# Performance work log

Measured on AMD Instinct MI355X. Metric: run time of the kernel, lower is better.

Reference implementation:

```python
import jax, jax.numpy as jnp
import numpy as np

IMAGE_DIM = 224


def setup_inputs() -> dict:
    key = jax.random.key(0)
    k1, k2, k3, k4, k5 = jax.random.split(key, 5)
    N, H, W = 64, IMAGE_DIM, IMAGE_DIM
    im1 = jax.random.normal(k1, (N, 3, H, W), dtype=jnp.float32)
    im2 = jax.random.normal(k2, (N, 3, H, W), dtype=jnp.float32)
    C = jax.random.normal(k3, (N, 2, H, W), dtype=jnp.float32)
    M1 = jax.random.uniform(k4, (N, 1, H, W), dtype=jnp.float32)
    M2 = jax.random.uniform(k5, (N, 1, H, W), dtype=jnp.float32)
    return {"im1": im1, "im2": im2, "C": C, "M1": M1, "M2": M2}


def _grid(dtype):
    # q = [repeat(arange(H), W), tile(arange(W), H)], shape [2, H*W]
    x = jnp.repeat(jnp.arange(IMAGE_DIM), IMAGE_DIM)
    y = jnp.tile(jnp.arange(IMAGE_DIM), IMAGE_DIM)
    return jnp.stack([x, y]).astype(dtype)  # [2, HW]


def _bilinear_sample(imflat, qi):
    # imflat: [N, 3, HW], qi: [N, 2, HW] float coords
    HW = imflat.shape[-1]
    px, py = qi[:, 0], qi[:, 1]  # [N, HW]
    fx, cx = jnp.floor(px), jnp.ceil(px)
    fy, cy = jnp.floor(py), jnp.ceil(py)

    def gather_pixel(nx, ny):
        # weight = prod over axes of (1 - |point - neighbor|)
        w = (1.0 - jnp.abs(px - nx)) * (1.0 - jnp.abs(py - ny))  # [N, HW]
        ind = (nx + IMAGE_DIM * ny).astype(jnp.int32)
        ind = jnp.clip(ind, 0, HW - 1)  # guard against out-of-range neighbors
        pix = jnp.take_along_axis(imflat, ind[:, None, :], axis=2)  # [N, 3, HW]
        return w[:, None, :] * pix

    return (gather_pixel(fx, fy) + gather_pixel(cx, fy)
            + gather_pixel(fx, cy) + gather_pixel(cy * 0 + cx, cy))


def reference(im1, im2, C, M1, M2):
    N, ch, H, W = im1.shape
    HW = H * W
    q = _grid(im1.dtype)[None]              # [1, 2, HW]
    Cflat = C.reshape(N, 2, HW)
    a = _bilinear_sample(im1.reshape(N, ch, HW), q + Cflat).reshape(N, ch, H, W) * M1
    b = _bilinear_sample(im2.reshape(N, ch, HW), q - Cflat).reshape(N, ch, H, W) * M2
    return a + b
```

## Files before the change

### kernel.cpp

```cpp
#include <hip/hip_runtime.h>

#define IMG 224
#define HW (IMG * IMG)
#define TILE 32
#define PAD 4
#define REG (TILE + 2 * PAD)
#define RSA 41
#define TABA (REG * RSA)
#define RSB 44
#define TABB (REG * RSB)

#define NXCD 8
#define NWG  (49 * 64)

typedef float vfloat4 __attribute__((ext_vector_type(4)));

__global__ __launch_bounds__(256, 4) void vm_kernel(
    const float* __restrict__ im1, const float* __restrict__ im2,
    const float* __restrict__ C, const float* __restrict__ M1,
    const float* __restrict__ M2, float* __restrict__ out)
{
    __shared__ float2 tabA[2 * TABA];
    __shared__ float  tabB[2 * TABB];

    const int bid     = blockIdx.x;
    const int logical = (bid & (NXCD - 1)) * (NWG / NXCD) + (bid >> 3);
    const int n       = logical / 49;
    const int tile    = logical - n * 49;

    const int x0   = (tile / 7) * TILE;
    const int y0   = (tile % 7) * TILE;
    const int t    = threadIdx.x;
    const int xlo  = x0 - PAD;
    const int ylo  = y0 - PAD;
    const int gbase = xlo + IMG * ylo;

    const float* i1n = im1 + (size_t)n * 3 * HW;
    const float* i2n = im2 + (size_t)n * 3 * HW;
    const float* Cn  = C  + (size_t)n * 2 * HW;
    const float* M1n = M1 + (size_t)n * HW;
    const float* M2n = M2 + (size_t)n * HW;

#pragma unroll
    for (int img = 0; img < 2; ++img) {
        const float* src = img ? i2n : i1n;
        float2* TA = tabA + img * TABA;
        float*  TB = tabB + img * TABB;
#pragma unroll
        for (int k = 0; k < 2; ++k) {
            int e = t + 256 * k;
            if (e < 400) {
                int r = e / 10, s = e - r * 10;
                int gi = gbase + IMG * r + 4 * s;
                float4 a, b, c;
                if (gi >= 0 && gi <= HW - 4) {
                    a = *(const float4*)(src + gi);
                    b = *(const float4*)(src + HW + gi);
                    c = *(const float4*)(src + 2 * HW + gi);
                } else {
#pragma unroll
                    for (int i = 0; i < 4; ++i) {
                        int g = min(max(gi + i, 0), HW - 1);
                        ((float*)&a)[i] = src[g];
                        ((float*)&b)[i] = src[HW + g];
                        ((float*)&c)[i] = src[2 * HW + g];
                    }
                }
                float2* dA = TA + r * RSA + 4 * s;
                dA[0] = make_float2(a.x, b.x);
                dA[1] = make_float2(a.y, b.y);
                dA[2] = make_float2(a.z, b.z);
                dA[3] = make_float2(a.w, b.w);
                *(float4*)(TB + r * RSB + 4 * s) = c;
            }
        }
    }

    const int tx  = t >> 3;
    const int ty0 = (t & 7) * 4;
    const int p   = (x0 + tx) * IMG + (y0 + ty0);

    const vfloat4 c0v = __builtin_nontemporal_load((const vfloat4*)(Cn + p));
    const vfloat4 c1v = __builtin_nontemporal_load((const vfloat4*)(Cn + HW + p));
    const vfloat4 m1v = __builtin_nontemporal_load((const vfloat4*)(M1n + p));
    const vfloat4 m2v = __builtin_nontemporal_load((const vfloat4*)(M2n + p));

    __syncthreads();

    const float xf = (float)(x0 + tx);
    float acc0[4], acc1[4], acc2[4];

#pragma unroll
    for (int i = 0; i < 4; ++i) {
        const float yf  = (float)(y0 + ty0 + i);
        const float cc0 = c0v[i];
        const float cc1 = c1v[i];
        const float m1i = m1v[i];
        const float m2i = m2v[i];
        float r0c, r1c, r2c;

        {
            float px = xf + cc0, py = yf + cc1;
            float fx = floorf(px), cx = ceilf(px);
            float fy = floorf(py), cy = ceilf(py);
            float wfx = 1.0f - (px - fx), wcx = 1.0f - (cx - px);
            float wfy = 1.0f - (py - fy), wcy = 1.0f - (cy - py);
            float w0 = wfx * wfy, w1 = wcx * wfy;
            float w2 = wfx * wcy, w3 = wcx * wcy;
            int gx0 = (int)fx, gy0 = (int)fy;
            int dx = (int)cx - gx0, dy = (int)cy - gy0;
            int q0 = gx0 - xlo, r0 = gy0 - ylo;
            int in = (q0 >= 0) & (q0 + dx <= REG - 1) &
                     (r0 >= 0) & (r0 + dy <= REG - 1);
            if (__all(in)) {
                int oA = r0 * RSA + q0;
                int oB = r0 * RSB + q0;
                float2 a0 = tabA[oA],            a1 = tabA[oA + dx];
                float2 a2 = tabA[oA + dy * RSA], a3 = tabA[oA + dx + dy * RSA];
                float  b0 = tabB[oB],            b1 = tabB[oB + dx];
                float  b2 = tabB[oB + dy * RSB], b3 = tabB[oB + dx + dy * RSB];
                r0c = m1i * (w0 * a0.x + w1 * a1.x + w2 * a2.x + w3 * a3.x);
                r1c = m1i * (w0 * a0.y + w1 * a1.y + w2 * a2.y + w3 * a3.y);
                r2c = m1i * (w0 * b0   + w1 * b1   + w2 * b2   + w3 * b3);
            } else {
                int i0 = min(max(gx0      + IMG * gy0,        0), HW - 1);
                int i1 = min(max(gx0 + dx + IMG * gy0,        0), HW - 1);
                int i2 = min(max(gx0      + IMG * (gy0 + dy), 0), HW - 1);
                int i3 = min(max(gx0 + dx + IMG * (gy0 + dy), 0), HW - 1);
                r0c = m1i * (w0 * i1n[i0] + w1 * i1n[i1] +
                             w2 * i1n[i2] + w3 * i1n[i3]);
                r1c = m1i * (w0 * i1n[HW + i0] + w1 * i1n[HW + i1] +
                             w2 * i1n[HW + i2] + w3 * i1n[HW + i3]);
                r2c = m1i * (w0 * i1n[2 * HW + i0] + w1 * i1n[2 * HW + i1] +
                             w2 * i1n[2 * HW + i2] + w3 * i1n[2 * HW + i3]);
            }
        }
        {
            float px = xf - cc0, py = yf - cc1;
            float fx = floorf(px), cx = ceilf(px);
            float fy = floorf(py), cy = ceilf(py);
            float wfx = 1.0f - (px - fx), wcx = 1.0f - (cx - px);
            float wfy = 1.0f - (py - fy), wcy = 1.0f - (cy - py);
            float w0 = wfx * wfy, w1 = wcx * wfy;
            float w2 = wfx * wcy, w3 = wcx * wcy;
            int gx0 = (int)fx, gy0 = (int)fy;
            int dx = (int)cx - gx0, dy = (int)cy - gy0;
            int q0 = gx0 - xlo, r0 = gy0 - ylo;
            int in = (q0 >= 0) & (q0 + dx <= REG - 1) &
                     (r0 >= 0) & (r0 + dy <= REG - 1);
            if (__all(in)) {
                const float2* TA = tabA + TABA;
                const float*  TB = tabB + TABB;
                int oA = r0 * RSA + q0;
                int oB = r0 * RSB + q0;
                float2 a0 = TA[oA],            a1 = TA[oA + dx];
                float2 a2 = TA[oA + dy * RSA], a3 = TA[oA + dx + dy * RSA];
                float  b0 = TB[oB],            b1 = TB[oB + dx];
                float  b2 = TB[oB + dy * RSB], b3 = TB[oB + dx + dy * RSB];
                r0c += m2i * (w0 * a0.x + w1 * a1.x + w2 * a2.x + w3 * a3.x);
                r1c += m2i * (w0 * a0.y + w1 * a1.y + w2 * a2.y + w3 * a3.y);
                r2c += m2i * (w0 * b0   + w1 * b1   + w2 * b2   + w3 * b3);
            } else {
                int i0 = min(max(gx0      + IMG * gy0,        0), HW - 1);
                int i1 = min(max(gx0 + dx + IMG * gy0,        0), HW - 1);
                int i2 = min(max(gx0      + IMG * (gy0 + dy), 0), HW - 1);
                int i3 = min(max(gx0 + dx + IMG * (gy0 + dy), 0), HW - 1);
                r0c += m2i * (w0 * i2n[i0] + w1 * i2n[i1] +
                              w2 * i2n[i2] + w3 * i2n[i3]);
                r1c += m2i * (w0 * i2n[HW + i0] + w1 * i2n[HW + i1] +
                              w2 * i2n[HW + i2] + w3 * i2n[HW + i3]);
                r2c += m2i * (w0 * i2n[2 * HW + i0] + w1 * i2n[2 * HW + i1] +
                              w2 * i2n[2 * HW + i2] + w3 * i2n[2 * HW + i3]);
            }
        }
        acc0[i] = r0c; acc1[i] = r1c; acc2[i] = r2c;
    }

    float* on = out + (size_t)n * 3 * HW;
    vfloat4 s0 = {acc0[0], acc0[1], acc0[2], acc0[3]};
    vfloat4 s1 = {acc1[0], acc1[1], acc1[2], acc1[3]};
    vfloat4 s2 = {acc2[0], acc2[1], acc2[2], acc2[3]};
    __builtin_nontemporal_store(s0, (vfloat4*)(on + p));
    __builtin_nontemporal_store(s1, (vfloat4*)(on + HW + p));
    __builtin_nontemporal_store(s2, (vfloat4*)(on + 2 * HW + p));
}

extern "C" void kernel_launch(void* const* d_in, const int* in_sizes, int n_in,
                              void* d_out, int out_size, void* d_ws, size_t ws_size,
                              hipStream_t stream) {
    const float* im1 = (const float*)d_in[0];
    const float* im2 = (const float*)d_in[1];
    const float* C   = (const float*)d_in[2];
    const float* M1  = (const float*)d_in[3];
    const float* M2  = (const float*)d_in[4];
    float* out = (float*)d_out;
    vm_kernel<<<dim3(NWG), 256, 0, stream>>>(im1, im2, C, M1, M2, out);
}
```

Before: 171.0 us.

## Process two tiles per block, prefetching second tile's loads during first compute

Each block now handles two consecutive tiles. The global loads for the second tile are issued into registers before the first tile is computed, then written to shared memory after a barrier, so memory latency overlaps with compute. The grid is halved and launch bounds drop to 3 waves per SIMD to make room for the extra registers the prefetch needs. The cost is higher register pressure, an extra barrier, and fewer blocks to cover the GPU.

After: 172.9 us. No clear change (+1.2%).

```diff
diff --git a/kernel.cpp b/kernel.cpp
--- a/kernel.cpp
+++ b/kernel.cpp
@@ -12,81 +12,47 @@
 
 #define NXCD 8
 #define NWG  (49 * 64)
+#define NBLK (NWG / 2)
 
 typedef float vfloat4 __attribute__((ext_vector_type(4)));
 
-__global__ __launch_bounds__(256, 4) void vm_kernel(
-    const float* __restrict__ im1, const float* __restrict__ im2,
-    const float* __restrict__ C, const float* __restrict__ M1,
-    const float* __restrict__ M2, float* __restrict__ out)
+struct Unit { float4 a, b, c; };
+
+__device__ __forceinline__ Unit load_unit(const float* __restrict__ src, int gi) {
+    Unit u;
+    if (gi >= 0 && gi <= HW - 4) {
+        u.a = *(const float4*)(src + gi);
+        u.b = *(const float4*)(src + HW + gi);
+        u.c = *(const float4*)(src + 2 * HW + gi);
+    } else {
+#pragma unroll
+        for (int i = 0; i < 4; ++i) {
+            int g = min(max(gi + i, 0), HW - 1);
+            ((float*)&u.a)[i] = src[g];
+            ((float*)&u.b)[i] = src[HW + g];
+            ((float*)&u.c)[i] = src[2 * HW + g];
+        }
+    }
+    return u;
+}
+
+__device__ __forceinline__ void write_unit(float2* TA, float* TB,
+                                           int r, int s, const Unit& u) {
+    float2* dA = TA + r * RSA + 4 * s;
+    dA[0] = make_float2(u.a.x, u.b.x);
+    dA[1] = make_float2(u.a.y, u.b.y);
+    dA[2] = make_float2(u.a.z, u.b.z);
+    dA[3] = make_float2(u.a.w, u.b.w);
+    *(float4*)(TB + r * RSB + 4 * s) = u.c;
+}
+
+__device__ __forceinline__ void compute_tile(
+    int x0, int y0, int xlo, int ylo, int tx, int ty0, int p,
+    const float2* __restrict__ tabA, const float* __restrict__ tabB,
+    vfloat4 c0v, vfloat4 c1v, vfloat4 m1v, vfloat4 m2v,
+    const float* __restrict__ i1n, const float* __restrict__ i2n,
+    float* __restrict__ on)
 {
-    __shared__ float2 tabA[2 * TABA];
-    __shared__ float  tabB[2 * TABB];
-
-    const int bid     = blockIdx.x;
-    const int logical = (bid & (NXCD - 1)) * (NWG / NXCD) + (bid >> 3);
-    const int n       = logical / 49;
-    const int tile    = logical - n * 49;
-
-    const int x0   = (tile / 7) * TILE;
-    const int y0   = (tile % 7) * TILE;
-    const int t    = threadIdx.x;
-    const int xlo  = x0 - PAD;
-    const int ylo  = y0 - PAD;
-    const int gbase = xlo + IMG * ylo;
-
-    const float* i1n = im1 + (size_t)n * 3 * HW;
-    const float* i2n = im2 + (size_t)n * 3 * HW;
-    const float* Cn  = C  + (size_t)n * 2 * HW;
-    const float* M1n = M1 + (size_t)n * HW;
-    const float* M2n = M2 + (size_t)n * HW;
-
-#pragma unroll
-    for (int img = 0; img < 2; ++img) {
-        const float* src = img ? i2n : i1n;
-        float2* TA = tabA + img * TABA;
-        float*  TB = tabB + img * TABB;
-#pragma unroll
-        for (int k = 0; k < 2; ++k) {
-            int e = t + 256 * k;
-            if (e < 400) {
-                int r = e / 10, s = e - r * 10;
-                int gi = gbase + IMG * r + 4 * s;
-                float4 a, b, c;
-                if (gi >= 0 && gi <= HW - 4) {
-                    a = *(const float4*)(src + gi);
-                    b = *(const float4*)(src + HW + gi);
-                    c = *(const float4*)(src + 2 * HW + gi);
-                } else {
-#pragma unroll
-                    for (int i = 0; i < 4; ++i) {
-                        int g = min(max(gi + i, 0), HW - 1);
-                        ((float*)&a)[i] = src[g];
-                        ((float*)&b)[i] = src[HW + g];
-                        ((float*)&c)[i] = src[2 * HW + g];
-                    }
-                }
-                float2* dA = TA + r * RSA + 4 * s;
-                dA[0] = make_float2(a.x, b.x);
-                dA[1] = make_float2(a.y, b.y);
-                dA[2] = make_float2(a.z, b.z);
-                dA[3] = make_float2(a.w, b.w);
-                *(float4*)(TB + r * RSB + 4 * s) = c;
-            }
-        }
-    }
-
-    const int tx  = t >> 3;
-    const int ty0 = (t & 7) * 4;
-    const int p   = (x0 + tx) * IMG + (y0 + ty0);
-
-    const vfloat4 c0v = __builtin_nontemporal_load((const vfloat4*)(Cn + p));
-    const vfloat4 c1v = __builtin_nontemporal_load((const vfloat4*)(Cn + HW + p));
-    const vfloat4 m1v = __builtin_nontemporal_load((const vfloat4*)(M1n + p));
-    const vfloat4 m2v = __builtin_nontemporal_load((const vfloat4*)(M2n + p));
-
-    __syncthreads();
-
     const float xf = (float)(x0 + tx);
     float acc0[4], acc1[4], acc2[4];
 
@@ -176,13 +142,105 @@
         acc0[i] = r0c; acc1[i] = r1c; acc2[i] = r2c;
     }
 
-    float* on = out + (size_t)n * 3 * HW;
     vfloat4 s0 = {acc0[0], acc0[1], acc0[2], acc0[3]};
     vfloat4 s1 = {acc1[0], acc1[1], acc1[2], acc1[3]};
     vfloat4 s2 = {acc2[0], acc2[1], acc2[2], acc2[3]};
     __builtin_nontemporal_store(s0, (vfloat4*)(on + p));
     __builtin_nontemporal_store(s1, (vfloat4*)(on + HW + p));
     __builtin_nontemporal_store(s2, (vfloat4*)(on + 2 * HW + p));
+}
+
+__global__ __launch_bounds__(256, 3) void vm_kernel(
+    const float* __restrict__ im1, const float* __restrict__ im2,
+    const float* __restrict__ C, const float* __restrict__ M1,
+    const float* __restrict__ M2, float* __restrict__ out)
+{
+    __shared__ float2 tabA[2 * TABA];
+    __shared__ float  tabB[2 * TABB];
+
+    const int bid = blockIdx.x;
+    const int swz = (bid & (NXCD - 1)) * (NBLK / NXCD) + (bid >> 3);
+    const int l0  = swz * 2;
+
+    const int t    = threadIdx.x;
+    const int tx   = t >> 3;
+    const int ty0  = (t & 7) * 4;
+    const bool has1 = (t < 144);
+    const int r0u = t / 10,         s0u = t - r0u * 10;
+    const int r1u = (t + 256) / 10, s1u = (t + 256) - r1u * 10;
+
+    const int n0  = l0 / 49, tl0 = l0 - n0 * 49;
+    const int x00 = (tl0 / 7) * TILE, y00 = (tl0 % 7) * TILE;
+    const int xlo0 = x00 - PAD, ylo0 = y00 - PAD;
+    const int gb0  = xlo0 + IMG * ylo0;
+    const float* i1n0 = im1 + (size_t)n0 * 3 * HW;
+    const float* i2n0 = im2 + (size_t)n0 * 3 * HW;
+    const float* Cn0  = C   + (size_t)n0 * 2 * HW;
+    const int p0 = (x00 + tx) * IMG + (y00 + ty0);
+
+    Unit u1a = load_unit(i1n0, gb0 + IMG * r0u + 4 * s0u);
+    Unit u2a = load_unit(i2n0, gb0 + IMG * r0u + 4 * s0u);
+    Unit u1b, u2b;
+    if (has1) {
+        u1b = load_unit(i1n0, gb0 + IMG * r1u + 4 * s1u);
+        u2b = load_unit(i2n0, gb0 + IMG * r1u + 4 * s1u);
+    }
+    const vfloat4 c0v0 = __builtin_nontemporal_load((const vfloat4*)(Cn0 + p0));
+    const vfloat4 c1v0 = __builtin_nontemporal_load((const vfloat4*)(Cn0 + HW + p0));
+    const vfloat4 m1v0 = __builtin_nontemporal_load(
+        (const vfloat4*)(M1 + (size_t)n0 * HW + p0));
+    const vfloat4 m2v0 = __builtin_nontemporal_load(
+        (const vfloat4*)(M2 + (size_t)n0 * HW + p0));
+
+    write_unit(tabA, tabB, r0u, s0u, u1a);
+    write_unit(tabA + TABA, tabB + TABB, r0u, s0u, u2a);
+    if (has1) {
+        write_unit(tabA, tabB, r1u, s1u, u1b);
+        write_unit(tabA + TABA, tabB + TABB, r1u, s1u, u2b);
+    }
+    __syncthreads();
+
+    const int l1  = l0 + 1;
+    const int n1  = l1 / 49, tl1 = l1 - n1 * 49;
+    const int x01 = (tl1 / 7) * TILE, y01 = (tl1 % 7) * TILE;
+    const int xlo1 = x01 - PAD, ylo1 = y01 - PAD;
+    const int gb1  = xlo1 + IMG * ylo1;
+    const float* i1n1 = im1 + (size_t)n1 * 3 * HW;
+    const float* i2n1 = im2 + (size_t)n1 * 3 * HW;
+    const float* Cn1  = C   + (size_t)n1 * 2 * HW;
+    const int p1 = (x01 + tx) * IMG + (y01 + ty0);
+
+    Unit v1a = load_unit(i1n1, gb1 + IMG * r0u + 4 * s0u);
+    Unit v2a = load_unit(i2n1, gb1 + IMG * r0u + 4 * s0u);
+    Unit v1b, v2b;
+    if (has1) {
+        v1b = load_unit(i1n1, gb1 + IMG * r1u + 4 * s1u);
+        v2b = load_unit(i2n1, gb1 + IMG * r1u + 4 * s1u);
+    }
+    const vfloat4 c0v1 = __builtin_nontemporal_load((const vfloat4*)(Cn1 + p1));
+    const vfloat4 c1v1 = __builtin_nontemporal_load((const vfloat4*)(Cn1 + HW + p1));
+    const vfloat4 m1v1 = __builtin_nontemporal_load(
+        (const vfloat4*)(M1 + (size_t)n1 * HW + p1));
+    const vfloat4 m2v1 = __builtin_nontemporal_load(
+        (const vfloat4*)(M2 + (size_t)n1 * HW + p1));
+
+    compute_tile(x00, y00, xlo0, ylo0, tx, ty0, p0, tabA, tabB,
+                 c0v0, c1v0, m1v0, m2v0, i1n0, i2n0,
+                 out + (size_t)n0 * 3 * HW);
+
+    __syncthreads();
+
+    write_unit(tabA, tabB, r0u, s0u, v1a);
+    write_unit(tabA + TABA, tabB + TABB, r0u, s0u, v2a);
+    if (has1) {
+        write_unit(tabA, tabB, r1u, s1u, v1b);
+        write_unit(tabA + TABA, tabB + TABB, r1u, s1u, v2b);
+    }
+    __syncthreads();
+
+    compute_tile(x01, y01, xlo1, ylo1, tx, ty0, p1, tabA, tabB,
+                 c0v1, c1v1, m1v1, m2v1, i1n1, i2n1,
+                 out + (size_t)n1 * 3 * HW);
 }
 
 extern "C" void kernel_launch(void* const* d_in, const int* in_sizes, int n_in,
@@ -194,5 +252,5 @@
     const float* M1  = (const float*)d_in[3];
     const float* M2  = (const float*)d_in[4];
     float* out = (float*)d_out;
-    vm_kernel<<<dim3(NWG), 256, 0, stream>>>(im1, im2, C, M1, M2, out);
-}
+    vm_kernel<<<dim3(NBLK), 256, 0, stream>>>(im1, im2, C, M1, M2, out);
+}
```

## Precompute gather offsets before barrier and software-pipeline LDS bilinear reads

Applied to the files above, without the earlier changes.

Moves the C/M loads ahead of the tile staging and computes all eight sample offsets and wave-uniform in-tile flags before the barrier, so that index math overlaps with global loads. After the barrier, LDS gathers for the next pixel are issued before the current pixel's weights are combined, which double-buffers the shared-memory reads. This raises register pressure (offset arrays plus two Gath sets in flight) under launch bounds of 4 blocks per SM, and the weights are recomputed twice.

New measurement: 189.8 us. 1.11x slower.

```diff
diff --git a/kernel.cpp b/kernel.cpp
--- a/kernel.cpp
+++ b/kernel.cpp
@@ -15,6 +15,21 @@
 
 typedef float vfloat4 __attribute__((ext_vector_type(4)));
 
+struct Gath { float2 a0, a1, a2, a3; float b0, b1, b2, b3; };
+
+__device__ __forceinline__ Gath issue_reads(
+    const float2* __restrict__ TA, const float* __restrict__ TB,
+    int oa, int ob, int dx, int dy)
+{
+    Gath g;
+    const int dA = dy * RSA, dB = dy * RSB;
+    g.a0 = TA[oa];           g.a1 = TA[oa + dx];
+    g.a2 = TA[oa + dA];      g.a3 = TA[oa + dx + dA];
+    g.b0 = TB[ob];           g.b1 = TB[ob + dx];
+    g.b2 = TB[ob + dB];      g.b3 = TB[ob + dx + dB];
+    return g;
+}
+
 __global__ __launch_bounds__(256, 4) void vm_kernel(
     const float* __restrict__ im1, const float* __restrict__ im2,
     const float* __restrict__ C, const float* __restrict__ M1,
@@ -40,6 +55,15 @@
     const float* Cn  = C  + (size_t)n * 2 * HW;
     const float* M1n = M1 + (size_t)n * HW;
     const float* M2n = M2 + (size_t)n * HW;
+
+    const int tx  = t >> 3;
+    const int ty0 = (t & 7) * 4;
+    const int p   = (x0 + tx) * IMG + (y0 + ty0);
+
+    const vfloat4 c0v = __builtin_nontemporal_load((const vfloat4*)(Cn + p));
+    const vfloat4 c1v = __builtin_nontemporal_load((const vfloat4*)(Cn + HW + p));
+    const vfloat4 m1v = __builtin_nontemporal_load((const vfloat4*)(M1n + p));
+    const vfloat4 m2v = __builtin_nontemporal_load((const vfloat4*)(M2n + p));
 
 #pragma unroll
     for (int img = 0; img < 2; ++img) {
@@ -76,104 +100,91 @@
         }
     }
 
-    const int tx  = t >> 3;
-    const int ty0 = (t & 7) * 4;
-    const int p   = (x0 + tx) * IMG + (y0 + ty0);
-
-    const vfloat4 c0v = __builtin_nontemporal_load((const vfloat4*)(Cn + p));
-    const vfloat4 c1v = __builtin_nontemporal_load((const vfloat4*)(Cn + HW + p));
-    const vfloat4 m1v = __builtin_nontemporal_load((const vfloat4*)(M1n + p));
-    const vfloat4 m2v = __builtin_nontemporal_load((const vfloat4*)(M2n + p));
-
-    __syncthreads();
-
     const float xf = (float)(x0 + tx);
-    float acc0[4], acc1[4], acc2[4];
-
+    int oAk[8], oBk[8], dxk[8], dyk[8], fak[8];
 #pragma unroll
     for (int i = 0; i < 4; ++i) {
-        const float yf  = (float)(y0 + ty0 + i);
-        const float cc0 = c0v[i];
-        const float cc1 = c1v[i];
-        const float m1i = m1v[i];
-        const float m2i = m2v[i];
-        float r0c, r1c, r2c;
-
-        {
-            float px = xf + cc0, py = yf + cc1;
-            float fx = floorf(px), cx = ceilf(px);
-            float fy = floorf(py), cy = ceilf(py);
-            float wfx = 1.0f - (px - fx), wcx = 1.0f - (cx - px);
-            float wfy = 1.0f - (py - fy), wcy = 1.0f - (cy - py);
-            float w0 = wfx * wfy, w1 = wcx * wfy;
-            float w2 = wfx * wcy, w3 = wcx * wcy;
-            int gx0 = (int)fx, gy0 = (int)fy;
-            int dx = (int)cx - gx0, dy = (int)cy - gy0;
+        const float yf = (float)(y0 + ty0 + i);
+#pragma unroll
+        for (int s2 = 0; s2 < 2; ++s2) {
+            const int k = i * 2 + s2;
+            const float sg = s2 ? -1.0f : 1.0f;
+            float px = xf + sg * c0v[i], py = yf + sg * c1v[i];
+            float fxf = floorf(px), cxf = ceilf(px);
+            float fyf = floorf(py), cyf = ceilf(py);
+            int gx0 = (int)fxf, gy0 = (int)fyf;
+            int dx = (int)cxf - gx0, dy = (int)cyf - gy0;
             int q0 = gx0 - xlo, r0 = gy0 - ylo;
             int in = (q0 >= 0) & (q0 + dx <= REG - 1) &
                      (r0 >= 0) & (r0 + dy <= REG - 1);
-            if (__all(in)) {
-                int oA = r0 * RSA + q0;
-                int oB = r0 * RSB + q0;
-                float2 a0 = tabA[oA],            a1 = tabA[oA + dx];
-                float2 a2 = tabA[oA + dy * RSA], a3 = tabA[oA + dx + dy * RSA];
-                float  b0 = tabB[oB],            b1 = tabB[oB + dx];
-                float  b2 = tabB[oB + dy * RSB], b3 = tabB[oB + dx + dy * RSB];
-                r0c = m1i * (w0 * a0.x + w1 * a1.x + w2 * a2.x + w3 * a3.x);
-                r1c = m1i * (w0 * a0.y + w1 * a1.y + w2 * a2.y + w3 * a3.y);
-                r2c = m1i * (w0 * b0   + w1 * b1   + w2 * b2   + w3 * b3);
+            int fa = __all(in);
+            fak[k] = fa;
+            oAk[k] = fa ? (r0 * RSA + q0) : 0;
+            oBk[k] = fa ? (r0 * RSB + q0) : 0;
+            dxk[k] = dx;
+            dyk[k] = dy;
+        }
+    }
+
+    __syncthreads();
+
+    float acc0[4], acc1[4], acc2[4];
+
+    Gath gA = issue_reads(tabA,        tabB,        oAk[0], oBk[0], dxk[0], dyk[0]);
+    Gath gB = issue_reads(tabA + TABA, tabB + TABB, oAk[1], oBk[1], dxk[1], dyk[1]);
+
+#pragma unroll
+    for (int i = 0; i < 4; ++i) {
+        Gath nA, nB;
+        if (i < 3) {
+            nA = issue_reads(tabA,        tabB,
+                             oAk[2 * i + 2], oBk[2 * i + 2],
+                             dxk[2 * i + 2], dyk[2 * i + 2]);
+            nB = issue_reads(tabA + TABA, tabB + TABB,
+                             oAk[2 * i + 3], oBk[2 * i + 3],
+                             dxk[2 * i + 3], dyk[2 * i + 3]);
+        }
+
+        const float yf = (float)(y0 + ty0 + i);
+        float r0c = 0.0f, r1c = 0.0f, r2c = 0.0f;
+
+#pragma unroll
+        for (int s2 = 0; s2 < 2; ++s2) {
+            const int k = i * 2 + s2;
+            const float mi = s2 ? m2v[i] : m1v[i];
+            const float sg = s2 ? -1.0f : 1.0f;
+            float px = xf + sg * c0v[i], py = yf + sg * c1v[i];
+            float fxf = floorf(px), cxf = ceilf(px);
+            float fyf = floorf(py), cyf = ceilf(py);
+            float wfx = 1.0f - (px - fxf), wcx = 1.0f - (cxf - px);
+            float wfy = 1.0f - (py - fyf), wcy = 1.0f - (cyf - py);
+            float w0 = wfx * wfy, w1 = wcx * wfy;
+            float w2 = wfx * wcy, w3 = wcx * wcy;
+
+            const Gath& g = s2 ? gB : gA;
+            if (fak[k]) {
+                r0c += mi * (w0 * g.a0.x + w1 * g.a1.x + w2 * g.a2.x + w3 * g.a3.x);
+                r1c += mi * (w0 * g.a0.y + w1 * g.a1.y + w2 * g.a2.y + w3 * g.a3.y);
+                r2c += mi * (w0 * g.b0   + w1 * g.b1   + w2 * g.b2   + w3 * g.b3);
             } else {
+                const float* src = s2 ? i2n : i1n;
+                int gx0 = (int)fxf, gy0 = (int)fyf;
+                int dx = (int)cxf - gx0, dy = (int)cyf - gy0;
                 int i0 = min(max(gx0      + IMG * gy0,        0), HW - 1);
                 int i1 = min(max(gx0 + dx + IMG * gy0,        0), HW - 1);
                 int i2 = min(max(gx0      + IMG * (gy0 + dy), 0), HW - 1);
                 int i3 = min(max(gx0 + dx + IMG * (gy0 + dy), 0), HW - 1);
-                r0c = m1i * (w0 * i1n[i0] + w1 * i1n[i1] +
-                             w2 * i1n[i2] + w3 * i1n[i3]);
-                r1c = m1i * (w0 * i1n[HW + i0] + w1 * i1n[HW + i1] +
-                             w2 * i1n[HW + i2] + w3 * i1n[HW + i3]);
-                r2c = m1i * (w0 * i1n[2 * HW + i0] + w1 * i1n[2 * HW + i1] +
-                             w2 * i1n[2 * HW + i2] + w3 * i1n[2 * HW + i3]);
+                r0c += mi * (w0 * src[i0] + w1 * src[i1] +
+                             w2 * src[i2] + w3 * src[i3]);
+                r1c += mi * (w0 * src[HW + i0] + w1 * src[HW + i1] +
+                             w2 * src[HW + i2] + w3 * src[HW + i3]);
+                r2c += mi * (w0 * src[2 * HW + i0] + w1 * src[2 * HW + i1] +
+                             w2 * src[2 * HW + i2] + w3 * src[2 * HW + i3]);
             }
         }
-        {
-            float px = xf - cc0, py = yf - cc1;
-            float fx = floorf(px), cx = ceilf(px);
-            float fy = floorf(py), cy = ceilf(py);
-            float wfx = 1.0f - (px - fx), wcx = 1.0f - (cx - px);
-            float wfy = 1.0f - (py - fy), wcy = 1.0f - (cy - py);
-            float w0 = wfx * wfy, w1 = wcx * wfy;
-            float w2 = wfx * wcy, w3 = wcx * wcy;
-            int gx0 = (int)fx, gy0 = (int)fy;
-            int dx = (int)cx - gx0, dy = (int)cy - gy0;
-            int q0 = gx0 - xlo, r0 = gy0 - ylo;
-            int in = (q0 >= 0) & (q0 + dx <= REG - 1) &
-                     (r0 >= 0) & (r0 + dy <= REG - 1);
-            if (__all(in)) {
-                const float2* TA = tabA + TABA;
-                const float*  TB = tabB + TABB;
-                int oA = r0 * RSA + q0;
-                int oB = r0 * RSB + q0;
-                float2 a0 = TA[oA],            a1 = TA[oA + dx];
-                float2 a2 = TA[oA + dy * RSA], a3 = TA[oA + dx + dy * RSA];
-                float  b0 = TB[oB],            b1 = TB[oB + dx];
-                float  b2 = TB[oB + dy * RSB], b3 = TB[oB + dx + dy * RSB];
-                r0c += m2i * (w0 * a0.x + w1 * a1.x + w2 * a2.x + w3 * a3.x);
-                r1c += m2i * (w0 * a0.y + w1 * a1.y + w2 * a2.y + w3 * a3.y);
-                r2c += m2i * (w0 * b0   + w1 * b1   + w2 * b2   + w3 * b3);
-            } else {
-                int i0 = min(max(gx0      + IMG * gy0,        0), HW - 1);
-                int i1 = min(max(gx0 + dx + IMG * gy0,        0), HW - 1);
-                int i2 = min(max(gx0      + IMG * (gy0 + dy), 0), HW - 1);
-                int i3 = min(max(gx0 + dx + IMG * (gy0 + dy), 0), HW - 1);
-                r0c += m2i * (w0 * i2n[i0] + w1 * i2n[i1] +
-                              w2 * i2n[i2] + w3 * i2n[i3]);
-                r1c += m2i * (w0 * i2n[HW + i0] + w1 * i2n[HW + i1] +
-                              w2 * i2n[HW + i2] + w3 * i2n[HW + i3]);
-                r2c += m2i * (w0 * i2n[2 * HW + i0] + w1 * i2n[2 * HW + i1] +
-                              w2 * i2n[2 * HW + i2] + w3 * i2n[2 * HW + i3]);
-            }
-        }
         acc0[i] = r0c; acc1[i] = r1c; acc2[i] = r2c;
+
+        gA = nA; gB = nB;
     }
 
     float* on = out + (size_t)n * 3 * HW;
```

## Enlarge tiles to 64x32 with 512-thread blocks to cut halo overhead

Applied to the files above, without the earlier changes.

Tiles become 64 rows by 32 columns, with a narrower 32-row tile at the last row band, and each block now runs 512 threads, giving 1792 blocks per launch. This lowers the ratio of staged halo to useful pixels in shared memory, so fewer redundant global loads feed the shared-memory tables. Staging now also starts after the C and mask loads are issued, letting them overlap. In exchange the block uses more shared memory (about 46KB), which may limit occupancy, and threads in the narrow edge tiles sit idle.

Result: no change. 169.5 us (-0.9%).

```diff
diff --git a/kernel.cpp b/kernel.cpp
--- a/kernel.cpp
+++ b/kernel.cpp
@@ -2,20 +2,67 @@
 
 #define IMG 224
 #define HW (IMG * IMG)
-#define TILE 32
+#define TLY 32
 #define PAD 4
-#define REG (TILE + 2 * PAD)
-#define RSA 41
-#define TABA (REG * RSA)
-#define RSB 44
-#define TABB (REG * RSB)
+#define REGY 40
+#define RSA 73
+#define TABA (REGY * RSA)
+#define RSB 76
+#define TABB (REGY * RSB)
 
 #define NXCD 8
-#define NWG  (49 * 64)
-
-typedef float vfloat4 __attribute__((ext_vector_type(4)));
-
-__global__ __launch_bounds__(256, 4) void vm_kernel(
+#define NBLK 1792
+
+typedef float vf4 __attribute__((ext_vector_type(4)));
+
+__device__ __forceinline__ void stage_unit(
+    const float* __restrict__ src, float2* __restrict__ TA,
+    float* __restrict__ TB, int gbase, int r, int s)
+{
+    int gi = gbase + IMG * r + 4 * s;
+    float4 a, b, c;
+    if (gi >= 0 && gi <= HW - 4) {
+        a = *(const float4*)(src + gi);
+        b = *(const float4*)(src + HW + gi);
+        c = *(const float4*)(src + 2 * HW + gi);
+    } else {
+#pragma unroll
+        for (int i = 0; i < 4; ++i) {
+            int g = min(max(gi + i, 0), HW - 1);
+            ((float*)&a)[i] = src[g];
+            ((float*)&b)[i] = src[HW + g];
+            ((float*)&c)[i] = src[2 * HW + g];
+        }
+    }
+    float2* dA = TA + r * RSA + 4 * s;
+    dA[0] = make_float2(a.x, b.x);
+    dA[1] = make_float2(a.y, b.y);
+    dA[2] = make_float2(a.z, b.z);
+    dA[3] = make_float2(a.w, b.w);
+    *(float4*)(TB + r * RSB + 4 * s) = c;
+}
+
+template <int SU>
+__device__ __forceinline__ void stage_all(
+    const float* __restrict__ i1n, const float* __restrict__ i2n,
+    float2* __restrict__ tabA, float* __restrict__ tabB, int gbase, int t)
+{
+    const int upi   = REGY * SU;
+    const int units = 2 * upi;
+#pragma unroll
+    for (int kk = 0; kk < 3; ++kk) {
+        int e = t + 512 * kk;
+        if (e < units) {
+            int img = (e >= upi);
+            int e2  = e - img * upi;
+            int r = e2 / SU, s = e2 - r * SU;
+            stage_unit(img ? i2n : i1n, tabA + img * TABA,
+                       tabB + img * TABB, gbase, r, s);
+        }
+    }
+}
+
+__global__ __launch_bounds__(512, 4) void vm_kernel(
     const float* __restrict__ im1, const float* __restrict__ im2,
     const float* __restrict__ C, const float* __restrict__ M1,
     const float* __restrict__ M2, float* __restrict__ out)
@@ -24,12 +71,16 @@
     __shared__ float  tabB[2 * TABB];
 
     const int bid     = blockIdx.x;
-    const int logical = (bid & (NXCD - 1)) * (NWG / NXCD) + (bid >> 3);
-    const int n       = logical / 49;
-    const int tile    = logical - n * 49;
-
-    const int x0   = (tile / 7) * TILE;
-    const int y0   = (tile % 7) * TILE;
+    const int logical = (bid & (NXCD - 1)) * (NBLK / NXCD) + (bid >> 3);
+    const int n       = logical / 28;
+    const int tile    = logical - n * 28;
+    const int xt      = tile / 7;
+    const int yt      = tile - xt * 7;
+    const int x0      = xt * 64;
+    const int y0      = yt * TLY;
+    const int w       = (xt == 3) ? 32 : 64;
+    const int cols    = w + 2 * PAD;
+
     const int t    = threadIdx.x;
     const int xlo  = x0 - PAD;
     const int ylo  = y0 - PAD;
@@ -41,148 +92,122 @@
     const float* M1n = M1 + (size_t)n * HW;
     const float* M2n = M2 + (size_t)n * HW;
 
-#pragma unroll
-    for (int img = 0; img < 2; ++img) {
-        const float* src = img ? i2n : i1n;
-        float2* TA = tabA + img * TABA;
-        float*  TB = tabB + img * TABB;
-#pragma unroll
-        for (int k = 0; k < 2; ++k) {
-            int e = t + 256 * k;
-            if (e < 400) {
-                int r = e / 10, s = e - r * 10;
-                int gi = gbase + IMG * r + 4 * s;
-                float4 a, b, c;
-                if (gi >= 0 && gi <= HW - 4) {
-                    a = *(const float4*)(src + gi);
-                    b = *(const float4*)(src + HW + gi);
-                    c = *(const float4*)(src + 2 * HW + gi);
-                } else {
-#pragma unroll
-                    for (int i = 0; i < 4; ++i) {
-                        int g = min(max(gi + i, 0), HW - 1);
-                        ((float*)&a)[i] = src[g];
-                        ((float*)&b)[i] = src[HW + g];
-                        ((float*)&c)[i] = src[2 * HW + g];
-                    }
-                }
-                float2* dA = TA + r * RSA + 4 * s;
-                dA[0] = make_float2(a.x, b.x);
-                dA[1] = make_float2(a.y, b.y);
-                dA[2] = make_float2(a.z, b.z);
-                dA[3] = make_float2(a.w, b.w);
-                *(float4*)(TB + r * RSB + 4 * s) = c;
-            }
-        }
-    }
-
     const int tx  = t >> 3;
     const int ty0 = (t & 7) * 4;
+    const bool act = (tx < w);
     const int p   = (x0 + tx) * IMG + (y0 + ty0);
 
-    const vfloat4 c0v = __builtin_nontemporal_load((const vfloat4*)(Cn + p));
-    const vfloat4 c1v = __builtin_nontemporal_load((const vfloat4*)(Cn + HW + p));
-    const vfloat4 m1v = __builtin_nontemporal_load((const vfloat4*)(M1n + p));
-    const vfloat4 m2v = __builtin_nontemporal_load((const vfloat4*)(M2n + p));
+    vf4 c0v, c1v, m1v, m2v;
+    if (act) {
+        c0v = __builtin_nontemporal_load((const vf4*)(Cn + p));
+        c1v = __builtin_nontemporal_load((const vf4*)(Cn + HW + p));
+        m1v = __builtin_nontemporal_load((const vf4*)(M1n + p));
+        m2v = __builtin_nontemporal_load((const vf4*)(M2n + p));
+    }
+
+    if (w == 64) stage_all<18>(i1n, i2n, tabA, tabB, gbase, t);
+    else         stage_all<10>(i1n, i2n, tabA, tabB, gbase, t);
 
     __syncthreads();
 
-    const float xf = (float)(x0 + tx);
-    float acc0[4], acc1[4], acc2[4];
+    if (act) {
+        const float xf = (float)(x0 + tx);
+        float acc0[4], acc1[4], acc2[4];
 
 #pragma unroll
-    for (int i = 0; i < 4; ++i) {
-        const float yf  = (float)(y0 + ty0 + i);
-        const float cc0 = c0v[i];
-        const float cc1 = c1v[i];
-        const float m1i = m1v[i];
-        const float m2i = m2v[i];
-        float r0c, r1c, r2c;
-
-        {
-            float px = xf + cc0, py = yf + cc1;
-            float fx = floorf(px), cx = ceilf(px);
-            float fy = floorf(py), cy = ceilf(py);
-            float wfx = 1.0f - (px - fx), wcx = 1.0f - (cx - px);
-            float wfy = 1.0f - (py - fy), wcy = 1.0f - (cy - py);
-            float w0 = wfx * wfy, w1 = wcx * wfy;
-            float w2 = wfx * wcy, w3 = wcx * wcy;
-            int gx0 = (int)fx, gy0 = (int)fy;
-            int dx = (int)cx - gx0, dy = (int)cy - gy0;
-            int q0 = gx0 - xlo, r0 = gy0 - ylo;
-            int in = (q0 >= 0) & (q0 + dx <= REG - 1) &
-                     (r0 >= 0) & (r0 + dy <= REG - 1);
-            if (__all(in)) {
-                int oA = r0 * RSA + q0;
-                int oB = r0 * RSB + q0;
-                float2 a0 = tabA[oA],            a1 = tabA[oA + dx];
-                float2 a2 = tabA[oA + dy * RSA], a3 = tabA[oA + dx + dy * RSA];
-                float  b0 = tabB[oB],            b1 = tabB[oB + dx];
-                float  b2 = tabB[oB + dy * RSB], b3 = tabB[oB + dx + dy * RSB];
-                r0c = m1i * (w0 * a0.x + w1 * a1.x + w2 * a2.x + w3 * a3.x);
-                r1c = m1i * (w0 * a0.y + w1 * a1.y + w2 * a2.y + w3 * a3.y);
-                r2c = m1i * (w0 * b0   + w1 * b1   + w2 * b2   + w3 * b3);
-            } else {
-                int i0 = min(max(gx0      + IMG * gy0,        0), HW - 1);
-                int i1 = min(max(gx0 + dx + IMG * gy0,        0), HW - 1);
-                int i2 = min(max(gx0      + IMG * (gy0 + dy), 0), HW - 1);
-                int i3 = min(max(gx0 + dx + IMG * (gy0 + dy), 0), HW - 1);
-                r0c = m1i * (w0 * i1n[i0] + w1 * i1n[i1] +
-                             w2 * i1n[i2] + w3 * i1n[i3]);
-                r1c = m1i * (w0 * i1n[HW + i0] + w1 * i1n[HW + i1] +
-                             w2 * i1n[HW + i2] + w3 * i1n[HW + i3]);
-                r2c = m1i * (w0 * i1n[2 * HW + i0] + w1 * i1n[2 * HW + i1] +
-                             w2 * i1n[2 * HW + i2] + w3 * i1n[2 * HW + i3]);
+        for (int i = 0; i < 4; ++i) {
+            const float yf  = (float)(y0 + ty0 + i);
+            const float cc0 = c0v[i];
+            const float cc1 = c1v[i];
+            const float m1i = m1v[i];
+            const float m2i = m2v[i];
+            float r0c, r1c, r2c;
+
+            {
+                float px = xf + cc0, py = yf + cc1;
+                float fx = floorf(px), cx = ceilf(px);
+                float fy = floorf(py), cy = ceilf(py);
+                float wfx = 1.0f - (px - fx), wcx = 1.0f - (cx - px);
+                float wfy = 1.0f - (py - fy), wcy = 1.0f - (cy - py);
+                float w0 = wfx * wfy, w1 = wcx * wfy;
+                float w2 = wfx * wcy, w3 = wcx * wcy;
+                int gx0 = (int)fx, gy0 = (int)fy;
+                int dx = (int)cx - gx0, dy = (int)cy - gy0;
+                int q0 = gx0 - xlo, r0 = gy0 - ylo;
+                int in = (q0 >= 0) & (q0 + dx <= cols - 1) &
+                         (r0 >= 0) & (r0 + dy <= REGY - 1);
+                if (__all(in)) {
+                    int oA = r0 * RSA + q0;
+                    int oB = r0 * RSB + q0;
+                    float2 a0 = tabA[oA],            a1 = tabA[oA + dx];
+                    float2 a2 = tabA[oA + dy * RSA], a3 = tabA[oA + dx + dy * RSA];
+                    float  b0 = tabB[oB],            b1 = tabB[oB + dx];
+                    float  b2 = tabB[oB + dy * RSB], b3 = tabB[oB + dx + dy * RSB];
+                    r0c = m1i * (w0 * a0.x + w1 * a1.x + w2 * a2.x + w3 * a3.x);
+                    r1c = m1i * (w0 * a0.y + w1 * a1.y + w2 * a2.y + w3 * a3.y);
+                    r2c = m1i * (w0 * b0   + w1 * b1   + w2 * b2   + w3 * b3);
+                } else {
+                    int i0 = min(max(gx0      + IMG * gy0,        0), HW - 1);
+                    int i1 = min(max(gx0 + dx + IMG * gy0,        0), HW - 1);
+                    int i2 = min(max(gx0      + IMG * (gy0 + dy), 0), HW - 1);
+                    int i3 = min(max(gx0 + dx + IMG * (gy0 + dy), 0), HW - 1);
+                    r0c = m1i * (w0 * i1n[i0] + w1 * i1n[i1] +
+                                 w2 * i1n[i2] + w3 * i1n[i3]);
+                    r1c = m1i * (w0 * i1n[HW + i0] + w1 * i1n[HW + i1] +
+                                 w2 * i1n[HW + i2] + w3 * i1n[HW + i3]);
+                    r2c = m1i * (w0 * i1n[2 * HW + i0] + w1 * i1n[2 * HW + i1] +
+                                 w2 * i1n[2 * HW + i2] + w3 * i1n[2 * HW + i3]);
+                }
             }
+            {
+                float px = xf - cc0, py = yf - cc1;
+                float fx = floorf(px), cx = ceilf(px);
+                float fy = floorf(py), cy = ceilf(py);
+                float wfx = 1.0f - (px - fx), wcx = 1.0f - (cx - px);
+                float wfy = 1.0f - (py - fy), wcy = 1.0f - (cy - py);
+                float w0 = wfx * wfy, w1 = wcx * wfy;
+                float w2 = wfx * wcy, w3 = wcx * wcy;
+                int gx0 = (int)fx, gy0 = (int)fy;
+                int dx = (int)cx - gx0, dy = (int)cy - gy0;
+                int q0 = gx0 - xlo, r0 = gy0 - ylo;
+                int in = (q0 >= 0) & (q0 + dx <= cols - 1) &
+                         (r0 >= 0) & (r0 + dy <= REGY - 1);
+                if (__all(in)) {
+                    const float2* TA = tabA + TABA;
+                    const float*  TB = tabB + TABB;
+                    int oA = r0 * RSA + q0;
+                    int oB = r0 * RSB + q0;
+                    float2 a0 = TA[oA],            a1 = TA[oA + dx];
+                    float2 a2 = TA[oA + dy * RSA], a3 = TA[oA + dx + dy * RSA];
+                    float  b0 = TB[oB],            b1 = TB[oB + dx];
+                    float  b2 = TB[oB + dy * RSB], b3 = TB[oB + dx + dy * RSB];
+                    r0c += m2i * (w0 * a0.x + w1 * a1.x + w2 * a2.x + w3 * a3.x);
+                    r1c += m2i * (w0 * a0.y + w1 * a1.y + w2 * a2.y + w3 * a3.y);
+                    r2c += m2i * (w0 * b0   + w1 * b1   + w2 * b2   + w3 * b3);
+                } else {
+                    int i0 = min(max(gx0      + IMG * gy0,        0), HW - 1);
+                    int i1 = min(max(gx0 + dx + IMG * gy0,        0), HW - 1);
+                    int i2 = min(max(gx0      + IMG * (gy0 + dy), 0), HW - 1);
+                    int i3 = min(max(gx0 + dx + IMG * (gy0 + dy), 0), HW - 1);
+                    r0c += m2i * (w0 * i2n[i0] + w1 * i2n[i1] +
+                                  w2 * i2n[i2] + w3 * i2n[i3]);
+                    r1c += m2i * (w0 * i2n[HW + i0] + w1 * i2n[HW + i1] +
+                                  w2 * i2n[HW + i2] + w3 * i2n[HW + i3]);
+                    r2c += m2i * (w0 * i2n[2 * HW + i0] + w1 * i2n[2 * HW + i1] +
+                                  w2 * i2n[2 * HW + i2] + w3 * i2n[2 * HW + i3]);
+                }
+            }
+            acc0[i] = r0c; acc1[i] = r1c; acc2[i] = r2c;
         }
-        {
-            float px = xf - cc0, py = yf - cc1;
-            float fx = floorf(px), cx = ceilf(px);
-            float fy = floorf(py), cy = ceilf(py);
-            float wfx = 1.0f - (px - fx), wcx = 1.0f - (cx - px);
-            float wfy = 1.0f - (py - fy), wcy = 1.0f - (cy - py);
-            float w0 = wfx * wfy, w1 = wcx * wfy;
-            float w2 = wfx * wcy, w3 = wcx * wcy;
-            int gx0 = (int)fx, gy0 = (int)fy;
-            int dx = (int)cx - gx0, dy = (int)cy - gy0;
-            int q0 = gx0 - xlo, r0 = gy0 - ylo;
-            int in = (q0 >= 0) & (q0 + dx <= REG - 1) &
-                     (r0 >= 0) & (r0 + dy <= REG - 1);
-            if (__all(in)) {
-                const float2* TA = tabA + TABA;
-                const float*  TB = tabB + TABB;
-                int oA = r0 * RSA + q0;
-                int oB = r0 * RSB + q0;
-                float2 a0 = TA[oA],            a1 = TA[oA + dx];
-                float2 a2 = TA[oA + dy * RSA], a3 = TA[oA + dx + dy * RSA];
-                float  b0 = TB[oB],            b1 = TB[oB + dx];
-                float  b2 = TB[oB + dy * RSB], b3 = TB[oB + dx + dy * RSB];
-                r0c += m2i * (w0 * a0.x + w1 * a1.x + w2 * a2.x + w3 * a3.x);
-                r1c += m2i * (w0 * a0.y + w1 * a1.y + w2 * a2.y + w3 * a3.y);
-                r2c += m2i * (w0 * b0   + w1 * b1   + w2 * b2   + w3 * b3);
-            } else {
-                int i0 = min(max(gx0      + IMG * gy0,        0), HW - 1);
-                int i1 = min(max(gx0 + dx + IMG * gy0,        0), HW - 1);
-                int i2 = min(max(gx0      + IMG * (gy0 + dy), 0), HW - 1);
-                int i3 = min(max(gx0 + dx + IMG * (gy0 + dy), 0), HW - 1);
-                r0c += m2i * (w0 * i2n[i0] + w1 * i2n[i1] +
-                              w2 * i2n[i2] + w3 * i2n[i3]);
-                r1c += m2i * (w0 * i2n[HW + i0] + w1 * i2n[HW + i1] +
-                              w2 * i2n[HW + i2] + w3 * i2n[HW + i3]);
-                r2c += m2i * (w0 * i2n[2 * HW + i0] + w1 * i2n[2 * HW + i1] +
-                              w2 * i2n[2 * HW + i2] + w3 * i2n[2 * HW + i3]);
-            }
-        }
-        acc0[i] = r0c; acc1[i] = r1c; acc2[i] = r2c;
-    }
-
-    float* on = out + (size_t)n * 3 * HW;
-    vfloat4 s0 = {acc0[0], acc0[1], acc0[2], acc0[3]};
-    vfloat4 s1 = {acc1[0], acc1[1], acc1[2], acc1[3]};
-    vfloat4 s2 = {acc2[0], acc2[1], acc2[2], acc2[3]};
-    __builtin_nontemporal_store(s0, (vfloat4*)(on + p));
-    __builtin_nontemporal_store(s1, (vfloat4*)(on + HW + p));
-    __builtin_nontemporal_store(s2, (vfloat4*)(on + 2 * HW + p));
+
+        float* on = out + (size_t)n * 3 * HW;
+        vf4 s0 = {acc0[0], acc0[1], acc0[2], acc0[3]};
+        vf4 s1 = {acc1[0], acc1[1], acc1[2], acc1[3]};
+        vf4 s2 = {acc2[0], acc2[1], acc2[2], acc2[3]};
+        __builtin_nontemporal_store(s0, (vf4*)(on + p));
+        __builtin_nontemporal_store(s1, (vf4*)(on + HW + p));
+        __builtin_nontemporal_store(s2, (vf4*)(on + 2 * HW + p));
+    }
 }
 
 extern "C" void kernel_launch(void* const* d_in, const int* in_sizes, int n_in,
@@ -194,5 +219,5 @@
     const float* M1  = (const float*)d_in[3];
     const float* M2  = (const float*)d_in[4];
     float* out = (float*)d_out;
-    vm_kernel<<<dim3(NWG), 256, 0, stream>>>(im1, im2, C, M1, M2, out);
-}
+    vm_kernel<<<dim3(NBLK), 512, 0, stream>>>(im1, im2, C, M1, M2, out);
+}
```
